# Kernel optimization log

Measured on AMD Instinct MI355X. Metric: run time of the kernel, lower is better.

The kernel has to match this reference:

```python
import jax, jax.numpy as jnp
import numpy as np

B, S, D, H = 2, 2048, 1024, 16
HD = D // H  # head_dim = 64


def setup_inputs() -> dict:
    key = jax.random.key(0)
    ks = jax.random.split(key, 6)
    scale = 1.0 / np.sqrt(D)
    x = jax.random.normal(ks[0], (B, S, D), dtype=jnp.float32)
    W_in = jax.random.normal(ks[1], (D, D), dtype=jnp.float32) * scale
    b_in = jnp.zeros((D,), dtype=jnp.float32)
    # per-head causal sequence-mixing weight, (H, S, S)
    W_mix = jax.random.normal(ks[2], (H, S, S), dtype=jnp.float32) / np.sqrt(S)
    W_out = jax.random.normal(ks[3], (D, D), dtype=jnp.float32) * scale
    b_out = jnp.zeros((D,), dtype=jnp.float32)
    index = S - 1  # python int; parallel form computes all indices at once
    return {"x": x, "W_in": W_in, "b_in": b_in, "W_mix": W_mix,
            "W_out": W_out, "b_out": b_out, "index": index}


def reference(x, W_in, b_in, W_mix, W_out, b_out, index):
    # in-projection (token-wise dense)
    xp = x @ W_in.T + b_in                      # (B, S, D)
    xh = xp.reshape(B, S, H, HD)                # split heads
    # causal (lower-triangular) per-head mixing over sequence positions
    causal = jnp.tril(jnp.ones((S, S), dtype=x.dtype))
    Wm = W_mix * causal                         # (H, S, S)
    # out[b,t,h,:] = sum_{j<=t} Wm[h,t,j] * xh[b,j,h,:]
    mixed = jnp.einsum('htj,bjhd->bthd', Wm, xh)
    out = mixed.reshape(B, S, D) @ W_out.T + b_out
    return out
```

## Files before the change

kernel.cpp:

```cpp
#include <hip/hip_runtime.h>
#include <hip/hip_bf16.h>
#include <stdint.h>

#define B_ 2
#define S_ 2048
#define D_ 1024
#define H_ 16
#define HD_ 64

typedef __attribute__((ext_vector_type(8))) short short8v;
typedef __attribute__((ext_vector_type(4))) float f32x4;
typedef __attribute__((ext_vector_type(4))) int int4v;

__device__ __forceinline__ unsigned short f2bf(float f) {
  union { float f; unsigned int u; } c; c.f = f;
  unsigned int u = c.u;
  unsigned int r = u + 0x7FFFu + ((u >> 16) & 1u);
  return (unsigned short)(r >> 16);
}

__global__ __launch_bounds__(256) void convert_f32_bf16(
    const float* __restrict__ in, unsigned short* __restrict__ out, int n4) {
  int i = blockIdx.x * 256 + threadIdx.x;
  if (i >= n4) return;
  float4 v = reinterpret_cast<const float4*>(in)[i];
  ushort4 o;
  o.x = f2bf(v.x); o.y = f2bf(v.y); o.z = f2bf(v.z); o.w = f2bf(v.w);
  reinterpret_cast<ushort4*>(out)[i] = o;
}

template<bool OUT_BF16>
__global__ __launch_bounds__(256) void gemm_bt(
    const unsigned short* __restrict__ A,
    const unsigned short* __restrict__ Bm,
    const float* __restrict__ bias,
    void* __restrict__ Cout,
    int M, int N, int K)
{
  __shared__ unsigned short As[128 * 40];
  __shared__ unsigned short Bs[128 * 40];
  const int tid = threadIdx.x;
  const int bM = blockIdx.y * 128, bN = blockIdx.x * 128;
  const int lane = tid & 63;
  const int wr = ((tid >> 7) & 1) * 64;
  const int wc = ((tid >> 6) & 1) * 64;
  const int lr = lane & 15, lk = (lane >> 4) * 8;
  const int srow = tid >> 1, skk = (tid & 1) * 16;

  f32x4 acc[4][4] = {};

  const size_t aBase = (size_t)(bM + srow) * K;
  const size_t bBase = (size_t)(bN + srow) * K;

  for (int k0 = 0; k0 < K; k0 += 32) {
    const int4v* asrc = reinterpret_cast<const int4v*>(A + aBase + k0 + skk);
    int4v* adst = reinterpret_cast<int4v*>(&As[srow * 40 + skk]);
    adst[0] = asrc[0]; adst[1] = asrc[1];
    const int4v* bsrc = reinterpret_cast<const int4v*>(Bm + bBase + k0 + skk);
    int4v* bdst = reinterpret_cast<int4v*>(&Bs[srow * 40 + skk]);
    bdst[0] = bsrc[0]; bdst[1] = bsrc[1];
    __syncthreads();
    short8v av[4], bv[4];
#pragma unroll
    for (int m = 0; m < 4; m++)
      av[m] = *reinterpret_cast<const short8v*>(&As[(wr + m * 16 + lr) * 40 + lk]);
#pragma unroll
    for (int n = 0; n < 4; n++)
      bv[n] = *reinterpret_cast<const short8v*>(&Bs[(wc + n * 16 + lr) * 40 + lk]);
#pragma unroll
    for (int m = 0; m < 4; m++)
#pragma unroll
      for (int n = 0; n < 4; n++)
        acc[m][n] = __builtin_amdgcn_mfma_f32_16x16x32_bf16(av[m], bv[n], acc[m][n], 0, 0, 0);
    __syncthreads();
  }

  const int r0 = wr + (lane >> 4) * 4;
  const int c0 = wc + lr;
#pragma unroll
  for (int m = 0; m < 4; m++) {
#pragma unroll
    for (int n = 0; n < 4; n++) {
      const int gc = bN + c0 + n * 16;
      const float bb = bias[gc];
#pragma unroll
      for (int j = 0; j < 4; j++) {
        const int gr = bM + r0 + m * 16 + j;
        float v = acc[m][n][j] + bb;
        if (OUT_BF16)
          reinterpret_cast<unsigned short*>(Cout)[(size_t)gr * N + gc] = f2bf(v);
        else
          reinterpret_cast<float*>(Cout)[(size_t)gr * N + gc] = v;
      }
    }
  }
}

__global__ __launch_bounds__(256) void transpose_heads(
    const unsigned short* __restrict__ xp,
    unsigned short* __restrict__ xhT)
{
  const int bh = blockIdx.y;
  const int t0 = blockIdx.x * 64;
  const int b = bh >> 4, h = bh & 15;
  __shared__ unsigned short tile[64][72];
  const int tid = threadIdx.x;
  const int c8 = (tid & 7) * 8;
  const int r = tid >> 3;
  const size_t inBase = ((size_t)(b * S_ + t0)) * D_ + h * HD_;
#pragma unroll
  for (int p = 0; p < 2; p++) {
    const int tt = r + p * 32;
    *reinterpret_cast<int4v*>(&tile[tt][c8]) =
        *reinterpret_cast<const int4v*>(&xp[inBase + (size_t)tt * D_ + c8]);
  }
  __syncthreads();
#pragma unroll
  for (int p = 0; p < 2; p++) {
    const int d = r + p * 32;
    short8v v;
#pragma unroll
    for (int i = 0; i < 8; i++) v[i] = (short)tile[c8 + i][d];
    *reinterpret_cast<short8v*>(&xhT[((size_t)(bh * HD_) + d) * S_ + t0 + c8]) = v;
  }
}

__global__ __launch_bounds__(256) void gemm_mix(
    const float* __restrict__ Wmix,
    const unsigned short* __restrict__ xhT,
    unsigned short* __restrict__ mixed)
{
  __shared__ unsigned short As[128 * 40];
  __shared__ unsigned short Bs[128 * 40];
  const int tid = threadIdx.x;
  const int h = blockIdx.y;
  const int T0 = blockIdx.x * 128;
  const int lane = tid & 63;
  const int wr = ((tid >> 7) & 1) * 64;
  const int wc = ((tid >> 6) & 1) * 64;
  const int lr = lane & 15, lk = (lane >> 4) * 8;
  const int srow = tid >> 1, skk = (tid & 1) * 16;

  f32x4 acc[4][4] = {};

  const int t = T0 + srow;
  const float* aRow = Wmix + ((size_t)h * S_ + t) * S_;
  const int c = srow;
  const int brow = ((c >> 6) * H_ + h) * HD_ + (c & 63);
  const unsigned short* bRow = xhT + (size_t)brow * S_;

  const int kMax = T0 + 128;
  for (int k0 = 0; k0 < kMax; k0 += 32) {
    union { unsigned short s[16]; int4v v[2]; } tmp;
#pragma unroll
    for (int q = 0; q < 4; q++) {
      float4 v = reinterpret_cast<const float4*>(aRow + k0 + skk)[q];
      const int jb = k0 + skk + q * 4;
      tmp.s[q * 4 + 0] = (jb + 0 <= t) ? f2bf(v.x) : (unsigned short)0;
      tmp.s[q * 4 + 1] = (jb + 1 <= t) ? f2bf(v.y) : (unsigned short)0;
      tmp.s[q * 4 + 2] = (jb + 2 <= t) ? f2bf(v.z) : (unsigned short)0;
      tmp.s[q * 4 + 3] = (jb + 3 <= t) ? f2bf(v.w) : (unsigned short)0;
    }
    int4v* adst = reinterpret_cast<int4v*>(&As[srow * 40 + skk]);
    adst[0] = tmp.v[0]; adst[1] = tmp.v[1];
    const int4v* bsrc = reinterpret_cast<const int4v*>(bRow + k0 + skk);
    int4v* bdst = reinterpret_cast<int4v*>(&Bs[srow * 40 + skk]);
    bdst[0] = bsrc[0]; bdst[1] = bsrc[1];
    __syncthreads();
    short8v av[4], bv[4];
#pragma unroll
    for (int m = 0; m < 4; m++)
      av[m] = *reinterpret_cast<const short8v*>(&As[(wr + m * 16 + lr) * 40 + lk]);
#pragma unroll
    for (int n = 0; n < 4; n++)
      bv[n] = *reinterpret_cast<const short8v*>(&Bs[(wc + n * 16 + lr) * 40 + lk]);
#pragma unroll
    for (int m = 0; m < 4; m++)
#pragma unroll
      for (int n = 0; n < 4; n++)
        acc[m][n] = __builtin_amdgcn_mfma_f32_16x16x32_bf16(av[m], bv[n], acc[m][n], 0, 0, 0);
    __syncthreads();
  }

  const int r0 = wr + (lane >> 4) * 4;
  const int c0 = wc + lr;
#pragma unroll
  for (int m = 0; m < 4; m++)
#pragma unroll
    for (int n = 0; n < 4; n++) {
      const int cc = c0 + n * 16;
      const int bb = cc >> 6, dd = cc & 63;
#pragma unroll
      for (int j = 0; j < 4; j++) {
        const int tt = T0 + r0 + m * 16 + j;
        mixed[((size_t)(bb * S_ + tt)) * D_ + h * HD_ + dd] = f2bf(acc[m][n][j]);
      }
    }
}

extern "C" void kernel_launch(void* const* d_in, const int* in_sizes, int n_in,
                              void* d_out, int out_size, void* d_ws, size_t ws_size,
                              hipStream_t stream) {
  const float* x     = (const float*)d_in[0];
  const float* W_in  = (const float*)d_in[1];
  const float* b_in  = (const float*)d_in[2];
  const float* W_mix = (const float*)d_in[3];
  const float* W_out = (const float*)d_in[4];
  const float* b_out = (const float*)d_in[5];

  char* ws = (char*)d_ws;
  unsigned short* xb    = (unsigned short*)(ws);
  unsigned short* xp    = (unsigned short*)(ws + 8u * 1024u * 1024u);
  unsigned short* wib   = (unsigned short*)(ws + 16u * 1024u * 1024u);
  unsigned short* wob   = (unsigned short*)(ws + 18u * 1024u * 1024u);
  unsigned short* xhT   = xb;
  unsigned short* mixed = xp;

  const int nX = B_ * S_ * D_ / 4;
  const int nW = D_ * D_ / 4;
  convert_f32_bf16<<<dim3((nX + 255) / 256), dim3(256), 0, stream>>>(x, xb, nX);
  convert_f32_bf16<<<dim3((nW + 255) / 256), dim3(256), 0, stream>>>(W_in, wib, nW);
  convert_f32_bf16<<<dim3((nW + 255) / 256), dim3(256), 0, stream>>>(W_out, wob, nW);

  gemm_bt<true><<<dim3(D_ / 128, B_ * S_ / 128), dim3(256), 0, stream>>>(
      xb, wib, b_in, (void*)xp, B_ * S_, D_, D_);

  transpose_heads<<<dim3(S_ / 64, B_ * H_), dim3(256), 0, stream>>>(xp, xhT);

  gemm_mix<<<dim3(S_ / 128, H_), dim3(256), 0, stream>>>(W_mix, xhT, mixed);

  gemm_bt<false><<<dim3(D_ / 128, B_ * S_ / 128), dim3(256), 0, stream>>>(
      mixed, wob, b_out, (void*)d_out, B_ * S_, D_, D_);
}
```

Baseline: 503.4 us.

## Use direct global-to-LDS loads, smaller causal mix tiles, and fuse conversions

```diff
diff --git a/kernel.cpp b/kernel.cpp
--- a/kernel.cpp
+++ b/kernel.cpp
@@ -19,14 +19,27 @@
   return (unsigned short)(r >> 16);
 }
 
-__global__ __launch_bounds__(256) void convert_f32_bf16(
-    const float* __restrict__ in, unsigned short* __restrict__ out, int n4) {
+__device__ __forceinline__ void gload16(const void* g, void* l) {
+  __builtin_amdgcn_global_load_lds(
+      (const __attribute__((address_space(1))) unsigned int*)g,
+      (__attribute__((address_space(3))) unsigned int*)l, 16, 0, 0);
+}
+
+#define NX4_ (B_ * S_ * D_ / 4)
+#define NW4_ (D_ * D_ / 4)
+__global__ __launch_bounds__(256) void convert3(
+    const float* __restrict__ x, const float* __restrict__ wi, const float* __restrict__ wo,
+    unsigned short* __restrict__ xb, unsigned short* __restrict__ wib,
+    unsigned short* __restrict__ wob) {
   int i = blockIdx.x * 256 + threadIdx.x;
-  if (i >= n4) return;
-  float4 v = reinterpret_cast<const float4*>(in)[i];
+  const float* src; unsigned short* dst; int j;
+  if (i < NX4_)              { src = x;  dst = xb;  j = i; }
+  else if (i < NX4_ + NW4_)  { src = wi; dst = wib; j = i - NX4_; }
+  else                       { src = wo; dst = wob; j = i - NX4_ - NW4_; }
+  float4 v = reinterpret_cast<const float4*>(src)[j];
   ushort4 o;
   o.x = f2bf(v.x); o.y = f2bf(v.y); o.z = f2bf(v.z); o.w = f2bf(v.w);
-  reinterpret_cast<ushort4*>(out)[i] = o;
+  reinterpret_cast<ushort4*>(dst)[j] = o;
 }
 
 template<bool OUT_BF16>
@@ -37,36 +50,33 @@
     void* __restrict__ Cout,
     int M, int N, int K)
 {
-  __shared__ unsigned short As[128 * 40];
-  __shared__ unsigned short Bs[128 * 40];
+  __shared__ unsigned short As[128 * 32];
+  __shared__ unsigned short Bs[128 * 32];
   const int tid = threadIdx.x;
   const int bM = blockIdx.y * 128, bN = blockIdx.x * 128;
   const int lane = tid & 63;
-  const int wr = ((tid >> 7) & 1) * 64;
-  const int wc = ((tid >> 6) & 1) * 64;
+  const int w = tid >> 6;
+  const int wr = (w >> 1) * 64;
+  const int wc = (w & 1) * 64;
   const int lr = lane & 15, lk = (lane >> 4) * 8;
-  const int srow = tid >> 1, skk = (tid & 1) * 16;
+  const int srA = w * 32 + (lane >> 2);
+  const int scs = (lane & 3) * 8;
 
   f32x4 acc[4][4] = {};
 
-  const size_t aBase = (size_t)(bM + srow) * K;
-  const size_t bBase = (size_t)(bN + srow) * K;
-
   for (int k0 = 0; k0 < K; k0 += 32) {
-    const int4v* asrc = reinterpret_cast<const int4v*>(A + aBase + k0 + skk);
-    int4v* adst = reinterpret_cast<int4v*>(&As[srow * 40 + skk]);
-    adst[0] = asrc[0]; adst[1] = asrc[1];
-    const int4v* bsrc = reinterpret_cast<const int4v*>(Bm + bBase + k0 + skk);
-    int4v* bdst = reinterpret_cast<int4v*>(&Bs[srow * 40 + skk]);
-    bdst[0] = bsrc[0]; bdst[1] = bsrc[1];
+    gload16(A + (size_t)(bM + srA) * K + k0 + scs,      &As[srA * 32 + scs]);
+    gload16(A + (size_t)(bM + srA + 16) * K + k0 + scs, &As[(srA + 16) * 32 + scs]);
+    gload16(Bm + (size_t)(bN + srA) * K + k0 + scs,      &Bs[srA * 32 + scs]);
+    gload16(Bm + (size_t)(bN + srA + 16) * K + k0 + scs, &Bs[(srA + 16) * 32 + scs]);
     __syncthreads();
     short8v av[4], bv[4];
 #pragma unroll
     for (int m = 0; m < 4; m++)
-      av[m] = *reinterpret_cast<const short8v*>(&As[(wr + m * 16 + lr) * 40 + lk]);
+      av[m] = *reinterpret_cast<const short8v*>(&As[(wr + m * 16 + lr) * 32 + lk]);
 #pragma unroll
     for (int n = 0; n < 4; n++)
-      bv[n] = *reinterpret_cast<const short8v*>(&Bs[(wc + n * 16 + lr) * 40 + lk]);
+      bv[n] = *reinterpret_cast<const short8v*>(&Bs[(wc + n * 16 + lr) * 32 + lk]);
 #pragma unroll
     for (int m = 0; m < 4; m++)
 #pragma unroll
@@ -125,67 +135,88 @@
   }
 }
 
+template<bool MASK>
+__device__ __forceinline__ short8v mix_fragA(const float* Asf, int rl, int lk, int k0, int T0) {
+  f32x4 f0 = *reinterpret_cast<const f32x4*>(&Asf[rl * 32 + lk]);
+  f32x4 f1 = *reinterpret_cast<const f32x4*>(&Asf[rl * 32 + lk + 4]);
+  const int t = T0 + rl;
+  short8v a;
+#pragma unroll
+  for (int e = 0; e < 4; e++) {
+    float v0 = f0[e], v1 = f1[e];
+    if (MASK) {
+      if (k0 + lk + e > t)     v0 = 0.0f;
+      if (k0 + lk + 4 + e > t) v1 = 0.0f;
+    }
+    a[e]     = (short)f2bf(v0);
+    a[4 + e] = (short)f2bf(v1);
+  }
+  return a;
+}
+
+template<bool MASK>
+__device__ __forceinline__ void mix_step(
+    const float* Asf, const unsigned short* Bs, f32x4 (&acc)[2][4],
+    int wr, int wc, int lr, int lk, int k0, int T0) {
+  short8v av[2], bv[4];
+#pragma unroll
+  for (int m = 0; m < 2; m++)
+    av[m] = mix_fragA<MASK>(Asf, wr + m * 16 + lr, lk, k0, T0);
+#pragma unroll
+  for (int n = 0; n < 4; n++)
+    bv[n] = *reinterpret_cast<const short8v*>(&Bs[(wc + n * 16 + lr) * 32 + lk]);
+#pragma unroll
+  for (int m = 0; m < 2; m++)
+#pragma unroll
+    for (int n = 0; n < 4; n++)
+      acc[m][n] = __builtin_amdgcn_mfma_f32_16x16x32_bf16(av[m], bv[n], acc[m][n], 0, 0, 0);
+}
+
 __global__ __launch_bounds__(256) void gemm_mix(
     const float* __restrict__ Wmix,
     const unsigned short* __restrict__ xhT,
     unsigned short* __restrict__ mixed)
 {
-  __shared__ unsigned short As[128 * 40];
-  __shared__ unsigned short Bs[128 * 40];
+  __shared__ float Asf[64 * 32];
+  __shared__ unsigned short Bs[128 * 32];
   const int tid = threadIdx.x;
   const int h = blockIdx.y;
-  const int T0 = blockIdx.x * 128;
+  const int xi = blockIdx.x;
+  const int tilei = (xi & 1) ? (31 - (xi >> 1)) : (xi >> 1);
+  const int T0 = tilei * 64;
   const int lane = tid & 63;
-  const int wr = ((tid >> 7) & 1) * 64;
-  const int wc = ((tid >> 6) & 1) * 64;
+  const int w = tid >> 6;
+  const int wr = (w >> 1) * 32;
+  const int wc = (w & 1) * 64;
   const int lr = lane & 15, lk = (lane >> 4) * 8;
-  const int srow = tid >> 1, skk = (tid & 1) * 16;
-
-  f32x4 acc[4][4] = {};
-
-  const int t = T0 + srow;
-  const float* aRow = Wmix + ((size_t)h * S_ + t) * S_;
-  const int c = srow;
-  const int brow = ((c >> 6) * H_ + h) * HD_ + (c & 63);
-  const unsigned short* bRow = xhT + (size_t)brow * S_;
-
-  const int kMax = T0 + 128;
+  const int arA = w * 16 + (lane >> 3);
+  const int acf = (lane & 7) * 4;
+  const int brA = w * 32 + (lane >> 2);
+  const int bcs = (lane & 3) * 8;
+  const int br0 = ((brA >> 6) * H_ + h) * HD_ + (brA & 63);
+  const int br1 = (((brA + 16) >> 6) * H_ + h) * HD_ + ((brA + 16) & 63);
+
+  f32x4 acc[2][4] = {};
+  const float* Wh = Wmix + (size_t)h * S_ * S_;
+
+  const int kMax = T0 + 64;
   for (int k0 = 0; k0 < kMax; k0 += 32) {
-    union { unsigned short s[16]; int4v v[2]; } tmp;
-#pragma unroll
-    for (int q = 0; q < 4; q++) {
-      float4 v = reinterpret_cast<const float4*>(aRow + k0 + skk)[q];
-      const int jb = k0 + skk + q * 4;
-      tmp.s[q * 4 + 0] = (jb + 0 <= t) ? f2bf(v.x) : (unsigned short)0;
-      tmp.s[q * 4 + 1] = (jb + 1 <= t) ? f2bf(v.y) : (unsigned short)0;
-      tmp.s[q * 4 + 2] = (jb + 2 <= t) ? f2bf(v.z) : (unsigned short)0;
-      tmp.s[q * 4 + 3] = (jb + 3 <= t) ? f2bf(v.w) : (unsigned short)0;
-    }
-    int4v* adst = reinterpret_cast<int4v*>(&As[srow * 40 + skk]);
-    adst[0] = tmp.v[0]; adst[1] = tmp.v[1];
-    const int4v* bsrc = reinterpret_cast<const int4v*>(bRow + k0 + skk);
-    int4v* bdst = reinterpret_cast<int4v*>(&Bs[srow * 40 + skk]);
-    bdst[0] = bsrc[0]; bdst[1] = bsrc[1];
-    __syncthreads();
-    short8v av[4], bv[4];
-#pragma unroll
-    for (int m = 0; m < 4; m++)
-      av[m] = *reinterpret_cast<const short8v*>(&As[(wr + m * 16 + lr) * 40 + lk]);
-#pragma unroll
-    for (int n = 0; n < 4; n++)
-      bv[n] = *reinterpret_cast<const short8v*>(&Bs[(wc + n * 16 + lr) * 40 + lk]);
-#pragma unroll
-    for (int m = 0; m < 4; m++)
-#pragma unroll
-      for (int n = 0; n < 4; n++)
-        acc[m][n] = __builtin_amdgcn_mfma_f32_16x16x32_bf16(av[m], bv[n], acc[m][n], 0, 0, 0);
+    gload16(Wh + (size_t)(T0 + arA) * S_ + k0 + acf,     &Asf[arA * 32 + acf]);
+    gload16(Wh + (size_t)(T0 + arA + 8) * S_ + k0 + acf, &Asf[(arA + 8) * 32 + acf]);
+    gload16(xhT + (size_t)br0 * S_ + k0 + bcs, &Bs[brA * 32 + bcs]);
+    gload16(xhT + (size_t)br1 * S_ + k0 + bcs, &Bs[(brA + 16) * 32 + bcs]);
+    __syncthreads();
+    if (k0 + 32 > T0)
+      mix_step<true>(Asf, Bs, acc, wr, wc, lr, lk, k0, T0);
+    else
+      mix_step<false>(Asf, Bs, acc, wr, wc, lr, lk, k0, T0);
     __syncthreads();
   }
 
   const int r0 = wr + (lane >> 4) * 4;
   const int c0 = wc + lr;
 #pragma unroll
-  for (int m = 0; m < 4; m++)
+  for (int m = 0; m < 2; m++)
 #pragma unroll
     for (int n = 0; n < 4; n++) {
       const int cc = c0 + n * 16;
@@ -216,18 +247,15 @@
   unsigned short* xhT   = xb;
   unsigned short* mixed = xp;
 
-  const int nX = B_ * S_ * D_ / 4;
-  const int nW = D_ * D_ / 4;
-  convert_f32_bf16<<<dim3((nX + 255) / 256), dim3(256), 0, stream>>>(x, xb, nX);
-  convert_f32_bf16<<<dim3((nW + 255) / 256), dim3(256), 0, stream>>>(W_in, wib, nW);
-  convert_f32_bf16<<<dim3((nW + 255) / 256), dim3(256), 0, stream>>>(W_out, wob, nW);
+  convert3<<<dim3((NX4_ + 2 * NW4_) / 256), dim3(256), 0, stream>>>(
+      x, W_in, W_out, xb, wib, wob);
 
   gemm_bt<true><<<dim3(D_ / 128, B_ * S_ / 128), dim3(256), 0, stream>>>(
       xb, wib, b_in, (void*)xp, B_ * S_, D_, D_);
 
   transpose_heads<<<dim3(S_ / 64, B_ * H_), dim3(256), 0, stream>>>(xp, xhT);
 
-  gemm_mix<<<dim3(S_ / 128, H_), dim3(256), 0, stream>>>(W_mix, xhT, mixed);
+  gemm_mix<<<dim3(S_ / 64, H_), dim3(256), 0, stream>>>(W_mix, xhT, mixed);
 
   gemm_bt<false><<<dim3(D_ / 128, B_ * S_ / 128), dim3(256), 0, stream>>>(
       mixed, wob, b_out, (void*)d_out, B_ * S_, D_, D_);
```

Measured after the change: 471.6 us. 6.3% less time.
